# Performance work log

Measured on AMD Instinct MI355X. Metric: run time of the kernel, lower is better.

## Reference

```python
import jax, jax.numpy as jnp
import numpy as np

B, NPG, K, H, G, L = 8, 128, 64, 600, 50, 6
N = B * NPG
CUTOFF = 10.0
BOX = 20.0
NUM_Z = 100


def setup_inputs() -> dict:
    key = jax.random.key(0)
    ks = jax.random.split(key, 16)
    s = 0.05
    z = jax.random.randint(ks[0], (N,), 0, 85)
    pos = jax.random.uniform(ks[1], (N, 3), dtype=jnp.float32) * BOX
    # weights stored as [in, out] (transposed torch Linear) so x @ w applies directly
    inp = {
        "z": z,
        "pos": pos,
        "embedding": jax.random.normal(ks[2], (NUM_Z, H), jnp.float32) * s,
        "mlp_w1": jax.random.normal(ks[3], (L, G, H), jnp.float32) * s,
        "mlp_b1": jnp.zeros((L, H), jnp.float32),
        "mlp_w2": jax.random.normal(ks[4], (L, H, H), jnp.float32) * s,
        "mlp_b2": jnp.zeros((L, H), jnp.float32),
        "lin1_w": jax.random.normal(ks[5], (L, H, H), jnp.float32) * s,  # CFConv lin1, no bias
        "lin2_w": jax.random.normal(ks[6], (L, H, H), jnp.float32) * s,
        "lin2_b": jnp.zeros((L, H), jnp.float32),
        "int_lin_w": jax.random.normal(ks[7], (L, H, H), jnp.float32) * s,
        "int_lin_b": jnp.zeros((L, H), jnp.float32),
        "pool_w": jax.random.normal(ks[8], (H, H), jnp.float32) * s,
        "pool_b": jnp.zeros((H,), jnp.float32),
    }
    return inp


def _ssp(x):
    # shifted softplus used by SchNet
    return jax.nn.softplus(x) - jnp.log(2.0)


def _build_graph(pos):
    # radius graph within each of the B graphs, capped at K neighbors per node
    posg = pos.reshape(B, NPG, 3)
    diff = posg[:, :, None, :] - posg[:, None, :, :]          # [B,n,n,3]
    dist2 = jnp.sum(diff * diff, axis=-1)                     # [B,n,n]
    eye = jnp.eye(NPG, dtype=bool)
    ok = (dist2 <= CUTOFF * CUTOFF) & (~eye)[None]
    neg = jnp.where(ok, -dist2, -jnp.inf)
    vals, idx = jax.lax.top_k(neg, K)                         # nearest K in-radius
    valid = jnp.isfinite(vals)                                # [B,n,K]
    nbr = idx + (jnp.arange(B) * NPG)[:, None, None]          # global node ids
    # recompute distances from gathered positions (differentiable, safe at masked slots)
    pos_nbr = pos[nbr.reshape(-1)].reshape(B, NPG, K, 3)
    dvec = posg[:, :, None, :] - pos_nbr
    dsq = jnp.sum(dvec * dvec, axis=-1)
    d = jnp.sqrt(jnp.where(valid, dsq, 1.0))
    d = jnp.where(valid, d, 0.0)                              # [B,n,K]
    return nbr, d, valid.astype(pos.dtype)


def reference(pos, embedding, mlp_w1, mlp_b1, mlp_w2, mlp_b2, lin1_w, lin2_w,
              lin2_b, int_lin_w, int_lin_b, pool_w, pool_b, z):
    nbr, d, valid = _build_graph(pos)
    nbr_flat = nbr.reshape(-1)

    # Gaussian smearing
    offs = jnp.linspace(0.0, CUTOFF, G)
    coeff = -0.5 / (offs[1] - offs[0]) ** 2
    edge_attr = jnp.exp(coeff * (d[..., None] - offs) ** 2)   # [B,n,K,G]
    # cosine cutoff, zero for invalid (padded) edges
    C = 0.5 * (jnp.cos(d * jnp.pi / CUTOFF) + 1.0) * valid    # [B,n,K]

    h = embedding[z]                                          # [N,H]
    for l in range(L):
        Wf = _ssp(edge_attr @ mlp_w1[l] + mlp_b1[l]) @ mlp_w2[l] + mlp_b2[l]
        Wf = Wf * C[..., None]                                # [B,n,K,H]
        x1 = h @ lin1_w[l]                                    # [N,H]
        xj = x1[nbr_flat].reshape(B, NPG, K, H)               # gather neighbors
        msg = jnp.sum(xj * Wf, axis=2).reshape(N, H)          # aggregate (add)
        m = msg @ lin2_w[l] + lin2_b[l]
        m = _ssp(m)
        m = m @ int_lin_w[l] + int_lin_b[l]
        h = h + m

    pooled = h.reshape(B, NPG, H).mean(axis=1)                # mean pool per graph
    return pooled @ pool_w + pool_b                           # [B, emb_dim]
```

## Files before the change

kernel.cpp:

```cpp
#include <hip/hip_runtime.h>
#include <cmath>

#define NB   8
#define NPG  128
#define NN   1024
#define KNB  64
#define HD   600
#define GG   50
#define LL   6
#define EE   (NN*KNB)
#define WROW 640
#define WCOL 608
#define NKNOT 1024

typedef __attribute__((ext_vector_type(8))) short short8;
typedef __attribute__((ext_vector_type(4))) short short4v;
typedef __attribute__((ext_vector_type(4))) float f32x4;

__device__ __forceinline__ short f2b(float f) {
  union { float f; unsigned u; } v; v.f = f;
  unsigned u = v.u;
  u += 0x7fffu + ((u >> 16) & 1u);
  return (short)(u >> 16);
}

__device__ __forceinline__ float b2f(unsigned us) {
  union { unsigned u; float f; } v; v.u = us << 16; return v.f;
}

__device__ __forceinline__ float ssp_fast(float x) {
  return fmaxf(x, 0.0f) + __logf(1.0f + __expf(-fabsf(x))) - 0.69314718055994531f;
}

__global__ __launch_bounds__(128) void build_graph_k(const float* __restrict__ pos,
        int* __restrict__ nbr, float* __restrict__ dist, float* __restrict__ cval) {
#pragma clang fp contract(off)
  __shared__ float d2s[128];
  __shared__ int scnt;
  int i = blockIdx.x;
  int li = i & 127;
  int base = i - li;
  int j = threadIdx.x;
  if (j == 0) scnt = 0;
  float px = pos[3*i], py = pos[3*i+1], pz = pos[3*i+2];
  int gj = base + j;
  float dx = px - pos[3*gj], dy = py - pos[3*gj+1], dz = pz - pos[3*gj+2];
  float d2 = dx*dx + dy*dy + dz*dz;
  bool valid = (j != li) && (d2 <= 100.0f);
  d2s[j] = valid ? d2 : 3.0e38f;
  __syncthreads();
  if (valid) {
    atomicAdd(&scnt, 1);
    int rank = 0;
    for (int j2 = 0; j2 < 128; ++j2) {
      float o = d2s[j2];
      rank += (o < d2 || (o == d2 && j2 < j)) ? 1 : 0;
    }
    if (rank < KNB) {
      int e = i*KNB + rank;
      nbr[e] = gj;
      float d = sqrtf(d2);
      dist[e] = d;
      cval[e] = 0.5f * (cosf(d * 0.31415926535897931f) + 1.0f);
    }
  }
  __syncthreads();
  int cnt = scnt; if (cnt > KNB) cnt = KNB;
  if (j < KNB && j >= cnt) {
    int e = i*KNB + j;
    nbr[e] = i; dist[e] = 0.0f; cval[e] = 0.0f;
  }
}

__global__ __launch_bounds__(256) void prep_k(const float* __restrict__ w1,
    short* __restrict__ basis, short* __restrict__ w1b) {
  int idx = blockIdx.x*256 + threadIdx.x;
  if (idx < NKNOT*64) {
    int i = idx >> 6, g = idx & 63;
    float v = 0.0f;
    if (g < GG) {
      const float step = 10.0f/49.0f;
      const float coeff = -0.5f/(step*step);
      float d = (float)i * (10.0f/(float)(NKNOT-1));
      float dd = d - step*(float)g;
      v = __expf(coeff*dd*dd);
    }
    basis[idx] = f2b(v);
  } else {
    int r = idx - NKNOT*64;
    if (r >= LL*WROW*64) return;
    int l = r / (WROW*64); int rem = r - l*WROW*64;
    int n = rem >> 6, k = rem & 63;
    float v = (n < HD && k < GG) ? w1[(size_t)l*GG*HD + (size_t)k*HD + n] : 0.0f;
    w1b[r] = f2b(v);
  }
}

__global__ __launch_bounds__(256) void conv_all_k(const float* __restrict__ l1w,
    const float* __restrict__ l2w, const float* __restrict__ ilw,
    const float* __restrict__ w2, short* __restrict__ dst) {
  __shared__ float T[64][65];
  int w = blockIdx.x;
  int kind = w / 6, l = w - kind*6;
  const float* s = (kind == 0) ? l1w : (kind == 1) ? l2w : (kind == 2) ? ilw : w2;
  s += (size_t)l*360000;
  int n0 = blockIdx.y*64, k0 = blockIdx.z*64;
  int tid = threadIdx.x;
  int ta = tid & 63, tb = tid >> 6;
  #pragma unroll
  for (int p = 0; p < 16; ++p) {
    int k = k0 + p*4 + tb;
    int n = n0 + ta;
    T[p*4 + tb][ta] = (k < HD && n < HD) ? s[(size_t)k*HD + n] : 0.0f;
  }
  __syncthreads();
  #pragma unroll
  for (int p = 0; p < 16; ++p) {
    int n = n0 + p*4 + tb;
    int k = k0 + ta;
    if (k < WCOL)
      dst[(size_t)w*WROW*WCOL + (size_t)n*WCOL + k] = f2b(T[ta][p*4 + tb]);
  }
}

__global__ __launch_bounds__(256) void embed_k(const int* __restrict__ z,
        const float* __restrict__ emb, float* __restrict__ h, short* __restrict__ hb) {
  int i = blockIdx.x;
  int zi = z[i];
  for (int j = threadIdx.x; j < WCOL; j += 256) {
    float v = (j < HD) ? emb[(size_t)zi*HD + j] : 0.0f;
    if (j < HD) h[(size_t)i*HD + j] = v;
    hb[(size_t)i*WCOL + j] = f2b(v);
  }
}

__global__ __launch_bounds__(256) void tabA_k(const short* __restrict__ basis,
    const short* __restrict__ w1b, const float* __restrict__ b1all,
    short* __restrict__ ttab_all) {
  const int MT = NKNOT/128;
  int l = blockIdx.x / MT;
  int mb = blockIdx.x - l*MT;
  const short* Bw = w1b + (size_t)l*WROW*64;
  short* outb = ttab_all + (size_t)l*NKNOT*WCOL;
  __shared__ __align__(16) short As[128*40];
  __shared__ __align__(16) short Bs[128*40];
  int tid = threadIdx.x;
  int lane = tid & 63, wv = tid >> 6;
  int wr = wv >> 1, wc = wv & 1;
  int col = lane & 15, quad = lane >> 4;
  int m0 = mb * 128;
  int n0 = blockIdx.y * 128;
  f32x4 acc[4][4] = {};
  for (int k0 = 0; k0 < 64; k0 += 32) {
    #pragma unroll
    for (int rep = 0; rep < 2; ++rep) {
      int s = tid + rep*256;
      int row = s >> 2, seg = s & 3;
      *(short8*)&As[row*40 + seg*8] =
          *(const short8*)(basis + (size_t)(m0 + row)*64 + k0 + seg*8);
      *(short8*)&Bs[row*40 + seg*8] =
          *(const short8*)(Bw + (size_t)(n0 + row)*64 + k0 + seg*8);
    }
    __syncthreads();
    short8 af[4], bf[4];
    #pragma unroll
    for (int mt = 0; mt < 4; ++mt)
      af[mt] = *(const short8*)&As[(wr*64 + mt*16 + col)*40 + quad*8];
    #pragma unroll
    for (int jt = 0; jt < 4; ++jt)
      bf[jt] = *(const short8*)&Bs[(wc*64 + jt*16 + col)*40 + quad*8];
    #pragma unroll
    for (int mt = 0; mt < 4; ++mt)
      #pragma unroll
      for (int jt = 0; jt < 4; ++jt)
        acc[mt][jt] = __builtin_amdgcn_mfma_f32_16x16x32_bf16(af[mt], bf[jt], acc[mt][jt], 0, 0, 0);
    __syncthreads();
  }
  #pragma unroll
  for (int jt = 0; jt < 4; ++jt) {
    int j = n0 + wc*64 + jt*16 + col;
    if (j >= WCOL) continue;
    float bj = (j < HD) ? b1all[(size_t)l*HD + j] : 0.0f;
    #pragma unroll
    for (int mt = 0; mt < 4; ++mt)
      #pragma unroll
      for (int r = 0; r < 4; ++r) {
        int row = m0 + wr*64 + mt*16 + quad*4 + r;
        short v = (j < HD) ? f2b(ssp_fast(acc[mt][jt][r] + bj)) : (short)0;
        outb[(size_t)row*WCOL + j] = v;
      }
  }
}

__global__ __launch_bounds__(256) void tabB_k(const short* __restrict__ ttab_all,
    const short* __restrict__ nwall, const float* __restrict__ b2all,
    short* __restrict__ wtab_b) {
  const int MT = NKNOT/128;
  int l = blockIdx.x / MT;
  int mb = blockIdx.x - l*MT;
  const short* A  = ttab_all + (size_t)l*NKNOT*WCOL;
  const short* Bw = nwall + (size_t)(18 + l)*WROW*WCOL;
  short* P = wtab_b + (size_t)l*NKNOT*HD;
  __shared__ __align__(16) short As[128*40];
  __shared__ __align__(16) short Bs[128*40];
  int tid = threadIdx.x;
  int lane = tid & 63, wv = tid >> 6;
  int wr = wv >> 1, wc = wv & 1;
  int col = lane & 15, quad = lane >> 4;
  int m0 = mb * 128;
  int n0 = blockIdx.y * 128;
  f32x4 acc[4][4] = {};
  for (int k0 = 0; k0 < WCOL; k0 += 32) {
    #pragma unroll
    for (int rep = 0; rep < 2; ++rep) {
      int s = tid + rep*256;
      int row = s >> 2, seg = s & 3;
      *(short8*)&As[row*40 + seg*8] =
          *(const short8*)(A + (size_t)(m0 + row)*WCOL + k0 + seg*8);
      *(short8*)&Bs[row*40 + seg*8] =
          *(const short8*)(Bw + (size_t)(n0 + row)*WCOL + k0 + seg*8);
    }
    __syncthreads();
    short8 af[4], bf[4];
    #pragma unroll
    for (int mt = 0; mt < 4; ++mt)
      af[mt] = *(const short8*)&As[(wr*64 + mt*16 + col)*40 + quad*8];
    #pragma unroll
    for (int jt = 0; jt < 4; ++jt)
      bf[jt] = *(const short8*)&Bs[(wc*64 + jt*16 + col)*40 + quad*8];
    #pragma unroll
    for (int mt = 0; mt < 4; ++mt)
      #pragma unroll
      for (int jt = 0; jt < 4; ++jt)
        acc[mt][jt] = __builtin_amdgcn_mfma_f32_16x16x32_bf16(af[mt], bf[jt], acc[mt][jt], 0, 0, 0);
    __syncthreads();
  }
  #pragma unroll
  for (int jt = 0; jt < 4; ++jt) {
    int j = n0 + wc*64 + jt*16 + col;
    if (j >= HD) continue;
    float bj = b2all[(size_t)l*HD + j];
    #pragma unroll
    for (int mt = 0; mt < 4; ++mt)
      #pragma unroll
      for (int r = 0; r < 4; ++r) {
        int row = m0 + wr*64 + mt*16 + quad*4 + r;
        P[(size_t)row*HD + j] = f2b(acc[mt][jt][r] + bj);
      }
  }
}

__global__ __launch_bounds__(192) void gather_k(const short* __restrict__ tabb,
    const float* __restrict__ cval, const int* __restrict__ nbr,
    const float* __restrict__ dist, const short* __restrict__ x1b,
    short* __restrict__ msgb) {
  __shared__ float cvs[64];
  __shared__ int nbs[64];
  __shared__ int tix[64];
  __shared__ float tfr[64];
  int node = blockIdx.x, tid = threadIdx.x;
  if (tid < 64) {
    int e = node*KNB + tid;
    cvs[tid] = cval[e];
    nbs[tid] = nbr[e];
    float u = dist[e] * ((float)(NKNOT-1)/10.0f);
    int i = (int)u;
    if (i > NKNOT-2) i = NKNOT-2;
    tix[tid] = i;
    tfr[tid] = u - (float)i;
  }
  __syncthreads();
  int j = tid*4;
  if (j >= WCOL) return;
  if (j >= HD) {
    *(uint2*)&msgb[(size_t)node*WCOL + j] = make_uint2(0u, 0u);
    return;
  }
  float s[4] = {0.f, 0.f, 0.f, 0.f};
  #pragma unroll 4
  for (int e = 0; e < KNB; ++e) {
    float Ce = cvs[e];
    if (Ce == 0.0f) continue;
    const short* w0 = tabb + (size_t)tix[e]*HD + j;
    float f = tfr[e];
    uint2 wa = *(const uint2*)w0;
    uint2 wb = *(const uint2*)(w0 + HD);
    uint2 xv = *(const uint2*)(x1b + (size_t)nbs[e]*WCOL + j);
    float a0 = b2f(wa.x & 0xffffu), a1 = b2f(wa.x >> 16);
    float a2 = b2f(wa.y & 0xffffu), a3 = b2f(wa.y >> 16);
    float b0 = b2f(wb.x & 0xffffu), b1 = b2f(wb.x >> 16);
    float b2v = b2f(wb.y & 0xffffu), b3 = b2f(wb.y >> 16);
    float x0 = b2f(xv.x & 0xffffu), x1v = b2f(xv.x >> 16);
    float x2 = b2f(xv.y & 0xffffu), x3 = b2f(xv.y >> 16);
    s[0] += Ce * (a0 + f*(b0 - a0)) * x0;
    s[1] += Ce * (a1 + f*(b1 - a1)) * x1v;
    s[2] += Ce * (a2 + f*(b2v - a2)) * x2;
    s[3] += Ce * (a3 + f*(b3 - a3)) * x3;
  }
  uint2 pack;
  pack.x = (unsigned)(unsigned short)f2b(s[0]) | ((unsigned)(unsigned short)f2b(s[1]) << 16);
  pack.y = (unsigned)(unsigned short)f2b(s[2]) | ((unsigned)(unsigned short)f2b(s[3]) << 16);
  *(uint2*)&msgb[(size_t)node*WCOL + j] = pack;
}

template<int MODE>
__global__ __launch_bounds__(512) void gemm_node_k(
    const short* __restrict__ A, const short* __restrict__ Bw,
    const float* __restrict__ bias, float* __restrict__ outf,
    short* __restrict__ outb, float* __restrict__ hacc) {
  __shared__ __align__(16) short As[2][2][32*40];
  __shared__ __align__(16) short Bs[2][2][64*40];
  __shared__ __align__(16) float red[256*8];
  int tid = threadIdx.x;
  int g = tid >> 8;
  int t = tid & 255;
  int lane = t & 63, wv = t >> 6;
  int col = lane & 15, quad = lane >> 4;
  int m0 = blockIdx.x * 32;
  int n0 = blockIdx.y * 64;
  int ar = t >> 3, aseg = t & 7;
  int br = t >> 2, bseg = t & 3;
  const int NST = g ? 9 : 10;
  const int kb  = g ? 320 : 0;
  const short* Aptr = A  + (size_t)(m0 + ar)*WCOL + kb + aseg*4;
  const short* Bptr = Bw + (size_t)(n0 + br)*WCOL + kb + bseg*8;
  f32x4 acc[2] = {};
  {
    short4v a0 = *(const short4v*)Aptr;
    short8  b0 = *(const short8*)Bptr;
    *(short4v*)&As[g][0][ar*40 + aseg*4] = a0;
    *(short8*)&Bs[g][0][br*40 + bseg*8] = b0;
  }
  __syncthreads();
  for (int kk = 0; kk < 10; ++kk) {
    int cur = kk & 1, nxt = cur ^ 1;
    short4v a_n; short8 b_n;
    if (kk + 1 < NST) {
      a_n = *(const short4v*)(Aptr + (kk + 1)*32);
      b_n = *(const short8*) (Bptr + (kk + 1)*32);
    }
    if (kk < NST) {
      short8 bf = *(const short8*)&Bs[g][cur][(wv*16 + col)*40 + quad*8];
      #pragma unroll
      for (int mt = 0; mt < 2; ++mt) {
        short8 af = *(const short8*)&As[g][cur][(mt*16 + col)*40 + quad*8];
        acc[mt] = __builtin_amdgcn_mfma_f32_16x16x32_bf16(af, bf, acc[mt], 0, 0, 0);
      }
    }
    if (kk + 1 < NST) {
      *(short4v*)&As[g][nxt][ar*40 + aseg*4] = a_n;
      *(short8*)&Bs[g][nxt][br*40 + bseg*8] = b_n;
    }
    __syncthreads();
  }
  if (g) {
    #pragma unroll
    for (int mt = 0; mt < 2; ++mt)
      *(f32x4*)&red[(t*2 + mt)*4] = acc[mt];
  }
  __syncthreads();
  if (g) return;
  #pragma unroll
  for (int mt = 0; mt < 2; ++mt)
    acc[mt] += *(const f32x4*)&red[(t*2 + mt)*4];
  int j = n0 + wv*16 + col;
  if (MODE == 0) {
    if (j < WCOL) {
      #pragma unroll
      for (int mt = 0; mt < 2; ++mt)
        #pragma unroll
        for (int r = 0; r < 4; ++r) {
          int row = m0 + mt*16 + quad*4 + r;
          outb[(size_t)row*WCOL + j] = (j < HD) ? f2b(acc[mt][r]) : (short)0;
        }
    }
  } else if (MODE == 1) {
    if (j < WCOL) {
      float bj = (j < HD) ? bias[j] : 0.0f;
      #pragma unroll
      for (int mt = 0; mt < 2; ++mt)
        #pragma unroll
        for (int r = 0; r < 4; ++r) {
          int row = m0 + mt*16 + quad*4 + r;
          outb[(size_t)row*WCOL + j] = (j < HD) ? f2b(ssp_fast(acc[mt][r] + bj)) : (short)0;
        }
    }
  } else {
    if (j < WCOL) {
      #pragma unroll
      for (int mt = 0; mt < 2; ++mt)
        #pragma unroll
        for (int r = 0; r < 4; ++r) {
          int row = m0 + mt*16 + quad*4 + r;
          if (j < HD) {
            float nv = hacc[(size_t)row*HD + j] + acc[mt][r] + bias[j];
            hacc[(size_t)row*HD + j] = nv;
            outb[(size_t)row*WCOL + j] = f2b(nv);
          } else {
            outb[(size_t)row*WCOL + j] = 0;
          }
        }
    }
  }
}

__global__ __launch_bounds__(256) void pool_mean_k(const float* __restrict__ h,
                                                   float* __restrict__ pooled) {
  __shared__ float red[4][64];
  int b = blockIdx.x;
  int cl = threadIdx.x & 63, q = threadIdx.x >> 6;
  int c = blockIdx.y*64 + cl;
  float s = 0.0f;
  if (c < HD) {
    int n0 = q*32;
    #pragma unroll 8
    for (int n = n0; n < n0 + 32; ++n)
      s += h[(size_t)(b*NPG + n)*HD + c];
  }
  red[q][cl] = s;
  __syncthreads();
  if (q == 0 && c < HD)
    pooled[(size_t)b*HD + c] =
        (red[0][cl] + red[1][cl] + red[2][cl] + red[3][cl]) * (1.0f/128.0f);
}

__global__ __launch_bounds__(256) void pool_out_k(const float* __restrict__ pooled,
    const float* __restrict__ pw, const float* __restrict__ pb,
    float* __restrict__ out) {
  __shared__ float red[4][64];
  int b = blockIdx.y;
  int tid = threadIdx.x;
  int jl = tid & 63, q = tid >> 6;
  int j = blockIdx.x*64 + jl;
  float s = 0.0f;
  if (j < HD) {
    int c0 = q*150, c1 = c0 + 150;
    for (int c = c0; c < c1; ++c)
      s += pooled[(size_t)b*HD + c] * pw[(size_t)c*HD + j];
  }
  red[q][jl] = s;
  __syncthreads();
  if (q == 0 && j < HD)
    out[(size_t)b*HD + j] = red[0][jl] + red[1][jl] + red[2][jl] + red[3][jl] + pb[j];
}

extern "C" void kernel_launch(void* const* d_in, const int* in_sizes, int n_in,
                              void* d_out, int out_size, void* d_ws, size_t ws_size,
                              hipStream_t stream) {
  const int*   z    = (const int*)d_in[0];
  const float* pos  = (const float*)d_in[1];
  const float* emb  = (const float*)d_in[2];
  const float* w1   = (const float*)d_in[3];
  const float* b1   = (const float*)d_in[4];
  const float* w2   = (const float*)d_in[5];
  const float* b2   = (const float*)d_in[6];
  const float* l1w  = (const float*)d_in[7];
  const float* l2w  = (const float*)d_in[8];
  const float* l2b  = (const float*)d_in[9];
  const float* ilw  = (const float*)d_in[10];
  const float* ilb  = (const float*)d_in[11];
  const float* pw   = (const float*)d_in[12];
  const float* pb   = (const float*)d_in[13];
  float* ws = (float*)d_ws;
  int*   nbr   = (int*)ws;
  float* cv    = ws + 65536;
  float* dist  = ws + 131072;
  float* pooled= ws + 196608;
  float* h     = ws + 204800;
  short* h_b   = (short*)(ws + 819200);
  short* msg_b = (short*)(ws + 1130496);
  short* mtmp_b= (short*)(ws + 1441792);
  short* x1_b  = (short*)(ws + 1753088);
  short* basis = (short*)(ws + 2064384);
  short* ttab  = (short*)(ws + 2097152);
  short* wtab_b= (short*)(ws + 3964928);
  short* w1b   = (short*)(ws + 5808128);
  short* nwall = (short*)(ws + 5931008);
  float* out   = (float*)d_out;

  const size_t WSZ = (size_t)WROW*WCOL;

  build_graph_k<<<NN, 128, 0, stream>>>(pos, nbr, dist, cv);
  prep_k<<<(NKNOT*64 + LL*WROW*64 + 255)/256, 256, 0, stream>>>(w1, basis, w1b);
  conv_all_k<<<dim3(24, 10, 10), 256, 0, stream>>>(l1w, l2w, ilw, w2, nwall);
  embed_k<<<NN, 256, 0, stream>>>(z, emb, h, h_b);

  tabA_k<<<dim3(LL*(NKNOT/128), 5), 256, 0, stream>>>(basis, w1b, b1, ttab);
  tabB_k<<<dim3(LL*(NKNOT/128), 5), 256, 0, stream>>>(ttab, nwall, b2, wtab_b);

  dim3 gn(32, 10);
  for (int l = 0; l < LL; ++l) {
    gemm_node_k<0><<<gn, 512, 0, stream>>>(h_b, nwall + (size_t)(0*6 + l)*WSZ,
        nullptr, nullptr, x1_b, nullptr);
    gather_k<<<NN, 192, 0, stream>>>(wtab_b + (size_t)l*NKNOT*HD, cv, nbr, dist, x1_b, msg_b);
    gemm_node_k<1><<<gn, 512, 0, stream>>>(msg_b, nwall + (size_t)(1*6 + l)*WSZ,
        l2b + (size_t)l*HD, nullptr, mtmp_b, nullptr);
    gemm_node_k<2><<<gn, 512, 0, stream>>>(mtmp_b, nwall + (size_t)(2*6 + l)*WSZ,
        ilb + (size_t)l*HD, nullptr, h_b, h);
  }
  pool_mean_k<<<dim3(NB, 10), 256, 0, stream>>>(h, pooled);
  pool_out_k<<<dim3(10, NB), 256, 0, stream>>>(pooled, pw, pb, out);
}
```

Measured before the change: 441.0 us.

## Merge prologue kernels into one launch and deepen GEMM K-tile to 64

```diff
diff --git a/kernel.cpp b/kernel.cpp
--- a/kernel.cpp
+++ b/kernel.cpp
@@ -10,7 +10,7 @@
 #define LL   6
 #define EE   (NN*KNB)
 #define WROW 640
-#define WCOL 608
+#define WCOL 640
 #define NKNOT 1024
 
 typedef __attribute__((ext_vector_type(8))) short short8;
@@ -32,105 +32,109 @@
   return fmaxf(x, 0.0f) + __logf(1.0f + __expf(-fabsf(x))) - 0.69314718055994531f;
 }
 
-__global__ __launch_bounds__(128) void build_graph_k(const float* __restrict__ pos,
-        int* __restrict__ nbr, float* __restrict__ dist, float* __restrict__ cval) {
+__global__ __launch_bounds__(256) void prolog_k(
+    const float* __restrict__ pos, int* __restrict__ nbr,
+    float* __restrict__ dist, float* __restrict__ cval,
+    const float* __restrict__ w1, short* __restrict__ basis, short* __restrict__ w1b,
+    const float* __restrict__ l1w, const float* __restrict__ l2w,
+    const float* __restrict__ ilw, const float* __restrict__ w2,
+    short* __restrict__ nwall,
+    const int* __restrict__ z, const float* __restrict__ emb,
+    float* __restrict__ h, short* __restrict__ hb) {
+  int bid = blockIdx.x;
+  int tid = threadIdx.x;
+  if (bid < 512) {
 #pragma clang fp contract(off)
-  __shared__ float d2s[128];
-  __shared__ int scnt;
-  int i = blockIdx.x;
-  int li = i & 127;
-  int base = i - li;
-  int j = threadIdx.x;
-  if (j == 0) scnt = 0;
-  float px = pos[3*i], py = pos[3*i+1], pz = pos[3*i+2];
-  int gj = base + j;
-  float dx = px - pos[3*gj], dy = py - pos[3*gj+1], dz = pz - pos[3*gj+2];
-  float d2 = dx*dx + dy*dy + dz*dz;
-  bool valid = (j != li) && (d2 <= 100.0f);
-  d2s[j] = valid ? d2 : 3.0e38f;
-  __syncthreads();
-  if (valid) {
-    atomicAdd(&scnt, 1);
-    int rank = 0;
-    for (int j2 = 0; j2 < 128; ++j2) {
-      float o = d2s[j2];
-      rank += (o < d2 || (o == d2 && j2 < j)) ? 1 : 0;
-    }
-    if (rank < KNB) {
-      int e = i*KNB + rank;
-      nbr[e] = gj;
-      float d = sqrtf(d2);
-      dist[e] = d;
-      cval[e] = 0.5f * (cosf(d * 0.31415926535897931f) + 1.0f);
-    }
-  }
-  __syncthreads();
-  int cnt = scnt; if (cnt > KNB) cnt = KNB;
-  if (j < KNB && j >= cnt) {
-    int e = i*KNB + j;
-    nbr[e] = i; dist[e] = 0.0f; cval[e] = 0.0f;
-  }
-}
-
-__global__ __launch_bounds__(256) void prep_k(const float* __restrict__ w1,
-    short* __restrict__ basis, short* __restrict__ w1b) {
-  int idx = blockIdx.x*256 + threadIdx.x;
-  if (idx < NKNOT*64) {
-    int i = idx >> 6, g = idx & 63;
-    float v = 0.0f;
-    if (g < GG) {
-      const float step = 10.0f/49.0f;
-      const float coeff = -0.5f/(step*step);
-      float d = (float)i * (10.0f/(float)(NKNOT-1));
-      float dd = d - step*(float)g;
-      v = __expf(coeff*dd*dd);
-    }
-    basis[idx] = f2b(v);
+    __shared__ float d2s[2][128];
+    __shared__ int scnt[2];
+    int sub = tid >> 7;
+    int j = tid & 127;
+    int i = bid*2 + sub;
+    int li = i & 127;
+    int base = i - li;
+    if (j == 0) scnt[sub] = 0;
+    float px = pos[3*i], py = pos[3*i+1], pz = pos[3*i+2];
+    int gj = base + j;
+    float dx = px - pos[3*gj], dy = py - pos[3*gj+1], dz = pz - pos[3*gj+2];
+    float d2 = dx*dx + dy*dy + dz*dz;
+    bool valid = (j != li) && (d2 <= 100.0f);
+    d2s[sub][j] = valid ? d2 : 3.0e38f;
+    __syncthreads();
+    if (valid) {
+      atomicAdd(&scnt[sub], 1);
+      int rank = 0;
+      for (int j2 = 0; j2 < 128; ++j2) {
+        float o = d2s[sub][j2];
+        rank += (o < d2 || (o == d2 && j2 < j)) ? 1 : 0;
+      }
+      if (rank < KNB) {
+        int e = i*KNB + rank;
+        nbr[e] = gj;
+        float d = sqrtf(d2);
+        dist[e] = d;
+        cval[e] = 0.5f * (cosf(d * 0.31415926535897931f) + 1.0f);
+      }
+    }
+    __syncthreads();
+    int cnt = scnt[sub]; if (cnt > KNB) cnt = KNB;
+    if (j < KNB && j >= cnt) {
+      int e = i*KNB + j;
+      nbr[e] = i; dist[e] = 0.0f; cval[e] = 0.0f;
+    }
+  } else if (bid < 1728) {
+    int idx = (bid - 512)*256 + tid;
+    if (idx < NKNOT*64) {
+      int i = idx >> 6, g = idx & 63;
+      float v = 0.0f;
+      if (g < GG) {
+        const float step = 10.0f/49.0f;
+        const float coeff = -0.5f/(step*step);
+        float d = (float)i * (10.0f/(float)(NKNOT-1));
+        float dd = d - step*(float)g;
+        v = __expf(coeff*dd*dd);
+      }
+      basis[idx] = f2b(v);
+    } else {
+      int r = idx - NKNOT*64;
+      if (r < LL*WROW*64) {
+        int l = r / (WROW*64); int rem = r - l*WROW*64;
+        int n = rem >> 6, k = rem & 63;
+        float v = (n < HD && k < GG) ? w1[(size_t)l*GG*HD + (size_t)k*HD + n] : 0.0f;
+        w1b[r] = f2b(v);
+      }
+    }
+  } else if (bid < 4128) {
+    __shared__ float T[64][65];
+    int r = bid - 1728;
+    int w = r / 100; int rem = r - w*100;
+    int ny = rem / 10, nz = rem - ny*10;
+    int kind = w / 6, l = w - kind*6;
+    const float* s = (kind == 0) ? l1w : (kind == 1) ? l2w : (kind == 2) ? ilw : w2;
+    s += (size_t)l*360000;
+    int n0 = ny*64, k0 = nz*64;
+    int ta = tid & 63, tb = tid >> 6;
+    #pragma unroll
+    for (int p = 0; p < 16; ++p) {
+      int k = k0 + p*4 + tb;
+      int n = n0 + ta;
+      T[p*4 + tb][ta] = (k < HD && n < HD) ? s[(size_t)k*HD + n] : 0.0f;
+    }
+    __syncthreads();
+    #pragma unroll
+    for (int p = 0; p < 16; ++p) {
+      int n = n0 + p*4 + tb;
+      int k = k0 + ta;
+      if (k < WCOL)
+        nwall[(size_t)w*WROW*WCOL + (size_t)n*WCOL + k] = f2b(T[ta][p*4 + tb]);
+    }
   } else {
-    int r = idx - NKNOT*64;
-    if (r >= LL*WROW*64) return;
-    int l = r / (WROW*64); int rem = r - l*WROW*64;
-    int n = rem >> 6, k = rem & 63;
-    float v = (n < HD && k < GG) ? w1[(size_t)l*GG*HD + (size_t)k*HD + n] : 0.0f;
-    w1b[r] = f2b(v);
-  }
-}
-
-__global__ __launch_bounds__(256) void conv_all_k(const float* __restrict__ l1w,
-    const float* __restrict__ l2w, const float* __restrict__ ilw,
-    const float* __restrict__ w2, short* __restrict__ dst) {
-  __shared__ float T[64][65];
-  int w = blockIdx.x;
-  int kind = w / 6, l = w - kind*6;
-  const float* s = (kind == 0) ? l1w : (kind == 1) ? l2w : (kind == 2) ? ilw : w2;
-  s += (size_t)l*360000;
-  int n0 = blockIdx.y*64, k0 = blockIdx.z*64;
-  int tid = threadIdx.x;
-  int ta = tid & 63, tb = tid >> 6;
-  #pragma unroll
-  for (int p = 0; p < 16; ++p) {
-    int k = k0 + p*4 + tb;
-    int n = n0 + ta;
-    T[p*4 + tb][ta] = (k < HD && n < HD) ? s[(size_t)k*HD + n] : 0.0f;
-  }
-  __syncthreads();
-  #pragma unroll
-  for (int p = 0; p < 16; ++p) {
-    int n = n0 + p*4 + tb;
-    int k = k0 + ta;
-    if (k < WCOL)
-      dst[(size_t)w*WROW*WCOL + (size_t)n*WCOL + k] = f2b(T[ta][p*4 + tb]);
-  }
-}
-
-__global__ __launch_bounds__(256) void embed_k(const int* __restrict__ z,
-        const float* __restrict__ emb, float* __restrict__ h, short* __restrict__ hb) {
-  int i = blockIdx.x;
-  int zi = z[i];
-  for (int j = threadIdx.x; j < WCOL; j += 256) {
-    float v = (j < HD) ? emb[(size_t)zi*HD + j] : 0.0f;
-    if (j < HD) h[(size_t)i*HD + j] = v;
-    hb[(size_t)i*WCOL + j] = f2b(v);
+    int i = bid - 4128;
+    int zi = z[i];
+    for (int j = tid; j < WCOL; j += 256) {
+      float v = (j < HD) ? emb[(size_t)zi*HD + j] : 0.0f;
+      if (j < HD) h[(size_t)i*HD + j] = v;
+      hb[(size_t)i*WCOL + j] = f2b(v);
+    }
   }
 }
 
@@ -306,10 +310,10 @@
 template<int MODE>
 __global__ __launch_bounds__(512) void gemm_node_k(
     const short* __restrict__ A, const short* __restrict__ Bw,
-    const float* __restrict__ bias, float* __restrict__ outf,
+    const float* __restrict__ bias,
     short* __restrict__ outb, float* __restrict__ hacc) {
-  __shared__ __align__(16) short As[2][2][32*40];
-  __shared__ __align__(16) short Bs[2][2][64*40];
+  __shared__ __align__(16) short As[2][2][32*72];
+  __shared__ __align__(16) short Bs[2][2][64*72];
   __shared__ __align__(16) float red[256*8];
   int tid = threadIdx.x;
   int g = tid >> 8;
@@ -318,38 +322,42 @@
   int col = lane & 15, quad = lane >> 4;
   int m0 = blockIdx.x * 32;
   int n0 = blockIdx.y * 64;
-  int ar = t >> 3, aseg = t & 7;
-  int br = t >> 2, bseg = t & 3;
-  const int NST = g ? 9 : 10;
-  const int kb  = g ? 320 : 0;
-  const short* Aptr = A  + (size_t)(m0 + ar)*WCOL + kb + aseg*4;
-  const short* Bptr = Bw + (size_t)(n0 + br)*WCOL + kb + bseg*8;
+  int ar = t >> 3, aseg = (t & 7)*8;
+  int br = t >> 2, bseg = (t & 3)*16;
+  const int kb = g * 320;
+  const short* Aptr = A  + (size_t)(m0 + ar)*WCOL + kb + aseg;
+  const short* Bptr = Bw + (size_t)(n0 + br)*WCOL + kb + bseg;
   f32x4 acc[2] = {};
   {
-    short4v a0 = *(const short4v*)Aptr;
-    short8  b0 = *(const short8*)Bptr;
-    *(short4v*)&As[g][0][ar*40 + aseg*4] = a0;
-    *(short8*)&Bs[g][0][br*40 + bseg*8] = b0;
+    short8 a0 = *(const short8*)Aptr;
+    short8 b0 = *(const short8*)Bptr;
+    short8 b1 = *(const short8*)(Bptr + 8);
+    *(short8*)&As[g][0][ar*72 + aseg] = a0;
+    *(short8*)&Bs[g][0][br*72 + bseg] = b0;
+    *(short8*)&Bs[g][0][br*72 + bseg + 8] = b1;
   }
   __syncthreads();
-  for (int kk = 0; kk < 10; ++kk) {
+  for (int kk = 0; kk < 5; ++kk) {
     int cur = kk & 1, nxt = cur ^ 1;
-    short4v a_n; short8 b_n;
-    if (kk + 1 < NST) {
-      a_n = *(const short4v*)(Aptr + (kk + 1)*32);
-      b_n = *(const short8*) (Bptr + (kk + 1)*32);
-    }
-    if (kk < NST) {
-      short8 bf = *(const short8*)&Bs[g][cur][(wv*16 + col)*40 + quad*8];
+    short8 a_n, b_n0, b_n1;
+    if (kk < 4) {
+      a_n  = *(const short8*)(Aptr + (kk + 1)*64);
+      b_n0 = *(const short8*)(Bptr + (kk + 1)*64);
+      b_n1 = *(const short8*)(Bptr + (kk + 1)*64 + 8);
+    }
+    #pragma unroll
+    for (int kh = 0; kh < 2; ++kh) {
+      short8 bf = *(const short8*)&Bs[g][cur][(wv*16 + col)*72 + kh*32 + quad*8];
       #pragma unroll
       for (int mt = 0; mt < 2; ++mt) {
-        short8 af = *(const short8*)&As[g][cur][(mt*16 + col)*40 + quad*8];
+        short8 af = *(const short8*)&As[g][cur][(mt*16 + col)*72 + kh*32 + quad*8];
         acc[mt] = __builtin_amdgcn_mfma_f32_16x16x32_bf16(af, bf, acc[mt], 0, 0, 0);
       }
     }
-    if (kk + 1 < NST) {
-      *(short4v*)&As[g][nxt][ar*40 + aseg*4] = a_n;
-      *(short8*)&Bs[g][nxt][br*40 + bseg*8] = b_n;
+    if (kk < 4) {
+      *(short8*)&As[g][nxt][ar*72 + aseg] = a_n;
+      *(short8*)&Bs[g][nxt][br*72 + bseg] = b_n0;
+      *(short8*)&Bs[g][nxt][br*72 + bseg + 8] = b_n1;
     }
     __syncthreads();
   }
@@ -468,22 +476,20 @@
   float* pooled= ws + 196608;
   float* h     = ws + 204800;
   short* h_b   = (short*)(ws + 819200);
-  short* msg_b = (short*)(ws + 1130496);
-  short* mtmp_b= (short*)(ws + 1441792);
-  short* x1_b  = (short*)(ws + 1753088);
-  short* basis = (short*)(ws + 2064384);
-  short* ttab  = (short*)(ws + 2097152);
-  short* wtab_b= (short*)(ws + 3964928);
-  short* w1b   = (short*)(ws + 5808128);
-  short* nwall = (short*)(ws + 5931008);
+  short* msg_b = (short*)(ws + 1146880);
+  short* mtmp_b= (short*)(ws + 1474560);
+  short* x1_b  = (short*)(ws + 1802240);
+  short* basis = (short*)(ws + 2129920);
+  short* ttab  = (short*)(ws + 2162688);
+  short* wtab_b= (short*)(ws + 4128768);
+  short* w1b   = (short*)(ws + 5971968);
+  short* nwall = (short*)(ws + 6094848);
   float* out   = (float*)d_out;
 
   const size_t WSZ = (size_t)WROW*WCOL;
 
-  build_graph_k<<<NN, 128, 0, stream>>>(pos, nbr, dist, cv);
-  prep_k<<<(NKNOT*64 + LL*WROW*64 + 255)/256, 256, 0, stream>>>(w1, basis, w1b);
-  conv_all_k<<<dim3(24, 10, 10), 256, 0, stream>>>(l1w, l2w, ilw, w2, nwall);
-  embed_k<<<NN, 256, 0, stream>>>(z, emb, h, h_b);
+  prolog_k<<<5152, 256, 0, stream>>>(pos, nbr, dist, cv,
+      w1, basis, w1b, l1w, l2w, ilw, w2, nwall, z, emb, h, h_b);
 
   tabA_k<<<dim3(LL*(NKNOT/128), 5), 256, 0, stream>>>(basis, w1b, b1, ttab);
   tabB_k<<<dim3(LL*(NKNOT/128), 5), 256, 0, stream>>>(ttab, nwall, b2, wtab_b);
@@ -491,12 +497,12 @@
   dim3 gn(32, 10);
   for (int l = 0; l < LL; ++l) {
     gemm_node_k<0><<<gn, 512, 0, stream>>>(h_b, nwall + (size_t)(0*6 + l)*WSZ,
-        nullptr, nullptr, x1_b, nullptr);
+        nullptr, x1_b, nullptr);
     gather_k<<<NN, 192, 0, stream>>>(wtab_b + (size_t)l*NKNOT*HD, cv, nbr, dist, x1_b, msg_b);
     gemm_node_k<1><<<gn, 512, 0, stream>>>(msg_b, nwall + (size_t)(1*6 + l)*WSZ,
-        l2b + (size_t)l*HD, nullptr, mtmp_b, nullptr);
+        l2b + (size_t)l*HD, mtmp_b, nullptr);
     gemm_node_k<2><<<gn, 512, 0, stream>>>(mtmp_b, nwall + (size_t)(2*6 + l)*WSZ,
-        ilb + (size_t)l*HD, nullptr, h_b, h);
+        ilb + (size_t)l*HD, h_b, h);
   }
   pool_mean_k<<<dim3(NB, 10), 256, 0, stream>>>(h, pooled);
   pool_out_k<<<dim3(10, NB), 256, 0, stream>>>(pooled, pw, pb, out);
```

Result: faster. 413.3 us (-6.3%).
